# Performance work log

Measured on AMD Instinct MI355X. Metric: run time of the kernel, lower is better.

Reference implementation:

```python
import jax, jax.numpy as jnp
import numpy as np
import math

B, DG, P, DA = 512, 1024, 1024, 256
LN_EPS = 1e-5  # torch LayerNorm default
EPS = 1e-12


def _ln(x, g, b):
    mu = jnp.mean(x, axis=-1, keepdims=True)
    var = jnp.mean((x - mu) ** 2, axis=-1, keepdims=True)
    return (x - mu) * jax.lax.rsqrt(var + LN_EPS) * g + b


def setup_inputs() -> dict:
    key = jax.random.key(0)
    ks = jax.random.split(key, 16)
    s = lambda fan_in: 1.0 / math.sqrt(fan_in)
    return {
        "hg": jax.random.normal(ks[0], (B, DG), jnp.float32),
        "desc_2d": jax.random.normal(ks[1], (B, P), jnp.float32),
        "Wq": jax.random.uniform(ks[2], (DA, DG), jnp.float32, -s(DG), s(DG)),
        "bq": jnp.zeros((DA,), jnp.float32),
        "wk_val": jax.random.uniform(ks[3], (DA,), jnp.float32, -1.0, 1.0),
        "bk_val": jax.random.uniform(ks[4], (DA,), jnp.float32, -1.0, 1.0),
        "wv_val": jax.random.uniform(ks[5], (DA,), jnp.float32, -1.0, 1.0),
        "bv_val": jax.random.uniform(ks[6], (DA,), jnp.float32, -1.0, 1.0),
        "Ek": jax.random.normal(ks[7], (P, DA), jnp.float32),
        "Ev": jax.random.normal(ks[8], (P, DA), jnp.float32),
        "Uq": jax.random.uniform(ks[9], (DA, DA), jnp.float32, -s(DA), s(DA)),
        "Vk": jax.random.uniform(ks[10], (DA, DA), jnp.float32, -s(DA), s(DA)),
        "ln_q_g": jnp.ones((DA,), jnp.float32), "ln_q_b": jnp.zeros((DA,), jnp.float32),
        "ln_k_g": jnp.ones((DA,), jnp.float32), "ln_k_b": jnp.zeros((DA,), jnp.float32),
        "ln_v_g": jnp.ones((DA,), jnp.float32), "ln_v_b": jnp.zeros((DA,), jnp.float32),
    }


def reference(hg, desc_2d, Wq, bq, wk_val, bk_val, wv_val, bv_val, Ek, Ev, Uq, Vk,
              ln_q_g, ln_q_b, ln_k_g, ln_k_b, ln_v_g, ln_v_b):
    # dropout is inference-mode (identity)
    q = _ln(hg @ Wq.T + bq, ln_q_g, ln_q_b)                       # (B, DA)
    # scalar -> token proj plus id embedding
    k = desc_2d[:, :, None] * wk_val + bk_val + Ek[None]          # (B, P, DA)
    v = desc_2d[:, :, None] * wv_val + bv_val + Ev[None]
    k = _ln(k, ln_k_g, ln_k_b)
    v = _ln(v, ln_v_g, ln_v_b)
    q2 = q @ Uq.T                                                 # (B, DA)
    k2 = jnp.einsum('bpd,ed->bpe', k, Vk)                         # (B, P, DA)
    e = jnp.einsum('bpd,bd->bp', k2, q2) / math.sqrt(DA)          # (B, P)
    alpha = jax.nn.sigmoid(e)
    alpha = alpha / (jnp.sum(alpha, axis=1, keepdims=True) + EPS)
    c = jnp.einsum('bp,bpd->bd', alpha, v)                        # (B, DA)
    return c, alpha
```

## Files before the change

kernel.cpp:

```cpp
#include <hip/hip_runtime.h>
#include <math.h>

#define B 512
#define DG 1024
#define P 1024
#define DA 256
#define LDP 68
#define BP (B * P)
#define BD (B * DA)

__device__ __forceinline__ float block_reduce_sum(float v, volatile float* red) {
    #pragma unroll
    for (int off = 32; off > 0; off >>= 1) v += __shfl_down(v, off, 64);
    const int lane = threadIdx.x & 63, wid = threadIdx.x >> 6;
    __syncthreads();
    if (lane == 0) red[wid] = v;
    __syncthreads();
    return red[0] + red[1] + red[2] + red[3];
}
__device__ __forceinline__ float wsum(float v) {
    #pragma unroll
    for (int m = 32; m > 0; m >>= 1) v += __shfl_xor(v, m, 64);
    return v;
}

#define FMA16(a4, b4, acc)                                   \
    acc[0][0] = fmaf(a4.x, b4.x, acc[0][0]);                 \
    acc[0][1] = fmaf(a4.x, b4.y, acc[0][1]);                 \
    acc[0][2] = fmaf(a4.x, b4.z, acc[0][2]);                 \
    acc[0][3] = fmaf(a4.x, b4.w, acc[0][3]);                 \
    acc[1][0] = fmaf(a4.y, b4.x, acc[1][0]);                 \
    acc[1][1] = fmaf(a4.y, b4.y, acc[1][1]);                 \
    acc[1][2] = fmaf(a4.y, b4.z, acc[1][2]);                 \
    acc[1][3] = fmaf(a4.y, b4.w, acc[1][3]);                 \
    acc[2][0] = fmaf(a4.z, b4.x, acc[2][0]);                 \
    acc[2][1] = fmaf(a4.z, b4.y, acc[2][1]);                 \
    acc[2][2] = fmaf(a4.z, b4.z, acc[2][2]);                 \
    acc[2][3] = fmaf(a4.z, b4.w, acc[2][3]);                 \
    acc[3][0] = fmaf(a4.w, b4.x, acc[3][0]);                 \
    acc[3][1] = fmaf(a4.w, b4.y, acc[3][1]);                 \
    acc[3][2] = fmaf(a4.w, b4.z, acc[3][2]);                 \
    acc[3][3] = fmaf(a4.w, b4.w, acc[3][3]);

__device__ __forceinline__ void stage_T(const float* __restrict__ src, int ldk, int m0, int k0,
                                        int tid, float* sD) {
    const int m = tid >> 3, k4 = (tid & 7) * 4;
    #pragma unroll
    for (int pass = 0; pass < 2; ++pass) {
        int mm = m + pass * 32;
        float4 v = *reinterpret_cast<const float4*>(&src[(m0 + mm) * ldk + k0 + k4]);
        sD[(k4 + 0) * LDP + mm] = v.x; sD[(k4 + 1) * LDP + mm] = v.y;
        sD[(k4 + 2) * LDP + mm] = v.z; sD[(k4 + 3) * LDP + mm] = v.w;
    }
}
__device__ __forceinline__ void stage_N1(const float* __restrict__ src, int ldn, int k0, int n0,
                                         int tid, float* sD) {
    const int k = tid >> 4, n4 = (tid & 15) * 4;
    #pragma unroll
    for (int pass = 0; pass < 2; ++pass) {
        int kk = k + pass * 16;
        *reinterpret_cast<float4*>(&sD[kk * LDP + n4]) =
            *reinterpret_cast<const float4*>(&src[(k0 + kk) * ldn + n0 + n4]);
    }
}
__device__ __forceinline__ void mm_inner(const float* sA, const float* sB, int tid, float acc[4][4]) {
    const int ty4 = (tid >> 4) * 4, tx4 = (tid & 15) * 4;
    #pragma unroll
    for (int kk = 0; kk < 32; ++kk) {
        float4 a4 = *reinterpret_cast<const float4*>(&sA[kk * LDP + ty4]);
        float4 b4 = *reinterpret_cast<const float4*>(&sB[kk * LDP + tx4]);
        FMA16(a4, b4, acc)
    }
}

__device__ __forceinline__ void epilog_uw(float dot, float s,
                                          float mck, float Bk, float Ck,
                                          float Bv, float Cv,
                                          float mwk, float Ak, float Av,
                                          float Wg, float Cg, float G_, float Bb,
                                          float& u, float& w) {
    float var = fmaf(s, fmaf(s, Ak, 2.0f * Bk), Ck);
    float rstd = rsqrtf(var + 1e-5f);
    float mu = fmaf(s, mwk, mck);
    float e = (rstd * (fmaf(s, Wg, Cg) + dot - mu * G_) + Bb) * 0.0625f;
    u = 1.0f / (1.0f + expf(-e));
    float varv = fmaf(s, fmaf(s, Av, 2.0f * Bv), Cv);
    w = u * rsqrtf(varv + 1e-5f);
}

__global__ __launch_bounds__(256) void KA(const float* __restrict__ hg, const float* __restrict__ Wq,
                                          const float* __restrict__ Uq,
                                          const float* __restrict__ Ek, const float* __restrict__ Ev,
                                          const float* __restrict__ wk, const float* __restrict__ bk,
                                          const float* __restrict__ wv, const float* __restrict__ bv,
                                          float* __restrict__ qp, float* __restrict__ UqT,
                                          float* __restrict__ pst, float* __restrict__ scal4) {
    __shared__ __align__(16) float sA[32 * LDP];
    __shared__ __align__(16) float sB[32 * LDP];
    const int tid = threadIdx.x, t = blockIdx.x;
    const int ty4 = (tid >> 4) * 4, tx4 = (tid & 15) * 4;

    if (t < 256) {
        const int mt = t & 7, nt = (t >> 3) & 3, ks = t >> 5;
        const int b0 = mt * 64, d0 = nt * 64, kc = ks * 128;
        float acc[4][4] = {};
        for (int kt = 0; kt < 128; kt += 32) {
            stage_T(hg, DG, b0, kc + kt, tid, sA);
            stage_T(Wq, DG, d0, kc + kt, tid, sB);
            __syncthreads();
            mm_inner(sA, sB, tid, acc);
            __syncthreads();
        }
        float* outp = qp + ks * BD;
        #pragma unroll
        for (int i = 0; i < 4; ++i) {
            float4 o = make_float4(acc[i][0], acc[i][1], acc[i][2], acc[i][3]);
            *reinterpret_cast<float4*>(&outp[(b0 + ty4 + i) * DA + d0 + tx4]) = o;
        }
    } else if (t < 320) {
        const int b2 = t - 256;
        const int e0 = (b2 & 7) * 32, f0 = (b2 >> 3) * 32;
        const int col = tid & 31, row8 = tid >> 5;
        #pragma unroll
        for (int pass = 0; pass < 4; ++pass) {
            int r = row8 + pass * 8;
            sA[r * 33 + col] = Uq[(e0 + r) * DA + f0 + col];
        }
        __syncthreads();
        #pragma unroll
        for (int pass = 0; pass < 4; ++pass) {
            int r = row8 + pass * 8;
            UqT[(f0 + r) * DA + e0 + col] = sA[col * 33 + r];
        }
    } else {
        const int tp = t - 320;
        const int wid = tid >> 6, lane = tid & 63;
        const int p = tp * 4 + wid;
        const int d4 = lane * 4;
        const float inv = 1.0f / DA;
        float4 ek4 = *reinterpret_cast<const float4*>(&Ek[p * DA + d4]);
        float4 ev4 = *reinterpret_cast<const float4*>(&Ev[p * DA + d4]);
        float4 wk4 = *reinterpret_cast<const float4*>(&wk[d4]);
        float4 bk4 = *reinterpret_cast<const float4*>(&bk[d4]);
        float4 wv4 = *reinterpret_cast<const float4*>(&wv[d4]);
        float4 bv4 = *reinterpret_cast<const float4*>(&bv[d4]);
        float ck0 = bk4.x + ek4.x, ck1 = bk4.y + ek4.y, ck2 = bk4.z + ek4.z, ck3 = bk4.w + ek4.w;
        float cv0 = bv4.x + ev4.x, cv1 = bv4.y + ev4.y, cv2 = bv4.z + ev4.z, cv3 = bv4.w + ev4.w;
        float Sck  = wsum(ck0 + ck1 + ck2 + ck3);
        float Sck2 = wsum(ck0*ck0 + ck1*ck1 + ck2*ck2 + ck3*ck3);
        float Swck = wsum(wk4.x*ck0 + wk4.y*ck1 + wk4.z*ck2 + wk4.w*ck3);
        float Scv  = wsum(cv0 + cv1 + cv2 + cv3);
        float Scv2 = wsum(cv0*cv0 + cv1*cv1 + cv2*cv2 + cv3*cv3);
        float Swcv = wsum(wv4.x*cv0 + wv4.y*cv1 + wv4.z*cv2 + wv4.w*cv3);
        float Swk  = wsum(wk4.x + wk4.y + wk4.z + wk4.w);
        float Swv  = wsum(wv4.x + wv4.y + wv4.z + wv4.w);
        float mwk = Swk * inv, mwv = Swv * inv;
        float mck = Sck * inv, mcv = Scv * inv;
        if (lane == 0) {
            pst[0 * P + p] = mck;
            pst[1 * P + p] = Swck * inv - mwk * mck;
            pst[2 * P + p] = Sck2 * inv - mck * mck;
            pst[3 * P + p] = mcv;
            pst[4 * P + p] = Swcv * inv - mwv * mcv;
            pst[5 * P + p] = Scv2 * inv - mcv * mcv;
        }
        if (p == 0) {
            float Swk2 = wsum(wk4.x*wk4.x + wk4.y*wk4.y + wk4.z*wk4.z + wk4.w*wk4.w);
            float Swv2 = wsum(wv4.x*wv4.x + wv4.y*wv4.y + wv4.z*wv4.z + wv4.w*wv4.w);
            if (lane == 0) {
                scal4[0] = mwk;
                scal4[1] = Swk2 * inv - mwk * mwk;
                scal4[2] = mwv;
                scal4[3] = Swv2 * inv - mwv * mwv;
            }
        }
    }
}

__global__ __launch_bounds__(256) void KC(const float* __restrict__ qp, const float* __restrict__ bq,
                                          const float* __restrict__ gq, const float* __restrict__ bqln,
                                          const float* __restrict__ UqT, const float* __restrict__ Vk,
                                          const float* __restrict__ gk,
                                          const float* __restrict__ wk, const float* __restrict__ bk,
                                          const float* __restrict__ bkln,
                                          float* __restrict__ gr, float* __restrict__ bscal) {
    __shared__ __align__(16) float q_lds[DA];
    __shared__ __align__(16) float q2_lds[DA];
    __shared__ float red[4];
    const int b = blockIdx.x, d = threadIdx.x;
    float x = bq[d];
    #pragma unroll
    for (int ks = 0; ks < 8; ++ks) x += qp[ks * BD + b * DA + d];
    float mu = block_reduce_sum(x, red) * (1.0f / DA);
    float xc = x - mu;
    float var = block_reduce_sum(xc * xc, red) * (1.0f / DA);
    float qv = xc * rsqrtf(var + 1e-5f) * gq[d] + bqln[d];
    q_lds[d] = qv;
    __syncthreads();

    float q2 = 0.f;
    for (int f = 0; f < DA; f += 4) {
        float4 qf = *reinterpret_cast<const float4*>(&q_lds[f]);
        q2 = fmaf(qf.x, UqT[(f + 0) * DA + d], q2);
        q2 = fmaf(qf.y, UqT[(f + 1) * DA + d], q2);
        q2 = fmaf(qf.z, UqT[(f + 2) * DA + d], q2);
        q2 = fmaf(qf.w, UqT[(f + 3) * DA + d], q2);
    }
    q2_lds[d] = q2;
    __syncthreads();

    float r = 0.f;
    for (int e = 0; e < DA; e += 4) {
        float4 qe = *reinterpret_cast<const float4*>(&q2_lds[e]);
        r = fmaf(qe.x, Vk[(e + 0) * DA + d], r);
        r = fmaf(qe.y, Vk[(e + 1) * DA + d], r);
        r = fmaf(qe.z, Vk[(e + 2) * DA + d], r);
        r = fmaf(qe.w, Vk[(e + 3) * DA + d], r);
    }
    float grv = gk[d] * r;
    gr[b * DA + d] = grv;

    float Wg = block_reduce_sum(wk[d] * grv, red);
    float Cg = block_reduce_sum(bk[d] * grv, red);
    float G_ = block_reduce_sum(grv, red);
    float Bb = block_reduce_sum(bkln[d] * r, red);
    if (d == 0) {
        bscal[b] = Wg; bscal[B + b] = Cg;
        bscal[2 * B + b] = G_; bscal[3 * B + b] = Bb;
    }
}

__global__ __launch_bounds__(256) void KD(const float* __restrict__ gr, const float* __restrict__ Ek,
                                          float* __restrict__ epart) {
    __shared__ __align__(16) float sA[32 * LDP];
    __shared__ __align__(16) float sB[32 * LDP];
    const int tid = threadIdx.x, t = blockIdx.x;
    const int ty4 = (tid >> 4) * 4, tx4 = (tid & 15) * 4;
    const int mt = t & 7, nt = (t >> 3) & 15, ks = t >> 7;
    const int b0 = mt * 64, p0 = nt * 64, kc = ks * 128;
    float acc[4][4] = {};
    for (int kt = 0; kt < 128; kt += 32) {
        stage_T(gr, DA, b0, kc + kt, tid, sA);
        stage_T(Ek, DA, p0, kc + kt, tid, sB);
        __syncthreads();
        mm_inner(sA, sB, tid, acc);
        __syncthreads();
    }
    float* outp = epart + ks * BP;
    #pragma unroll
    for (int i = 0; i < 4; ++i) {
        float4 o = make_float4(acc[i][0], acc[i][1], acc[i][2], acc[i][3]);
        *reinterpret_cast<float4*>(&outp[(b0 + ty4 + i) * P + p0 + tx4]) = o;
    }
}

__global__ __launch_bounds__(256) void KF(const float* __restrict__ epart, const float* __restrict__ desc,
                                          const float* __restrict__ bscal, const float* __restrict__ pst,
                                          const float* __restrict__ scal4, const float* __restrict__ Ev,
                                          float* __restrict__ cpart) {
    __shared__ __align__(16) float sA[32 * LDP];
    __shared__ __align__(16) float sB[32 * LDP];
    const int tid = threadIdx.x, t = blockIdx.x;
    const int ty4 = (tid >> 4) * 4, tx4 = (tid & 15) * 4;
    const int mt = t & 7, nt = (t >> 3) & 3, ks = t >> 5;
    const int b0 = mt * 64, d0 = nt * 64, kc = ks * 128;
    const float mwk = scal4[0], Ak = scal4[1], Av = scal4[3];
    const int m = tid >> 3, k4 = (tid & 7) * 4;
    float acc[4][4] = {};
    for (int kt = 0; kt < 128; kt += 32) {
        const int kg = kc + kt;
        #pragma unroll
        for (int pass = 0; pass < 2; ++pass) {
            int mm = m + pass * 32;
            const int b = b0 + mm;
            const int p = kg + k4;
            float4 e0 = *reinterpret_cast<const float4*>(&epart[b * P + p]);
            float4 e1 = *reinterpret_cast<const float4*>(&epart[BP + b * P + p]);
            float4 s4 = *reinterpret_cast<const float4*>(&desc[b * P + p]);
            float4 mck4 = *reinterpret_cast<const float4*>(&pst[p]);
            float4 Bk4  = *reinterpret_cast<const float4*>(&pst[P + p]);
            float4 Ck4  = *reinterpret_cast<const float4*>(&pst[2 * P + p]);
            float4 Bv4  = *reinterpret_cast<const float4*>(&pst[4 * P + p]);
            float4 Cv4  = *reinterpret_cast<const float4*>(&pst[5 * P + p]);
            const float Wg = bscal[b], Cg = bscal[B + b];
            const float G_ = bscal[2 * B + b], Bb = bscal[3 * B + b];
            float u, w;
            epilog_uw(e0.x + e1.x, s4.x, mck4.x, Bk4.x, Ck4.x, Bv4.x, Cv4.x,
                      mwk, Ak, Av, Wg, Cg, G_, Bb, u, w);
            sA[(k4 + 0) * LDP + mm] = w;
            epilog_uw(e0.y + e1.y, s4.y, mck4.y, Bk4.y, Ck4.y, Bv4.y, Cv4.y,
                      mwk, Ak, Av, Wg, Cg, G_, Bb, u, w);
            sA[(k4 + 1) * LDP + mm] = w;
            epilog_uw(e0.z + e1.z, s4.z, mck4.z, Bk4.z, Ck4.z, Bv4.z, Cv4.z,
                      mwk, Ak, Av, Wg, Cg, G_, Bb, u, w);
            sA[(k4 + 2) * LDP + mm] = w;
            epilog_uw(e0.w + e1.w, s4.w, mck4.w, Bk4.w, Ck4.w, Bv4.w, Cv4.w,
                      mwk, Ak, Av, Wg, Cg, G_, Bb, u, w);
            sA[(k4 + 3) * LDP + mm] = w;
        }
        stage_N1(Ev, DA, kg, d0, tid, sB);
        __syncthreads();
        mm_inner(sA, sB, tid, acc);
        __syncthreads();
    }
    float* outp = cpart + ks * BD;
    #pragma unroll
    for (int i = 0; i < 4; ++i) {
        float4 o = make_float4(acc[i][0], acc[i][1], acc[i][2], acc[i][3]);
        *reinterpret_cast<float4*>(&outp[(b0 + ty4 + i) * DA + d0 + tx4]) = o;
    }
}

__global__ __launch_bounds__(256) void KG(const float* __restrict__ epart, const float* __restrict__ desc,
                                          const float* __restrict__ bscal, const float* __restrict__ pst,
                                          const float* __restrict__ scal4, const float* __restrict__ cpart,
                                          const float* __restrict__ gv, const float* __restrict__ wv,
                                          const float* __restrict__ bvv, const float* __restrict__ bvln,
                                          float* __restrict__ alpha_out, float* __restrict__ out_c) {
    __shared__ float red[4];
    const int b = blockIdx.x, tid = threadIdx.x;
    const float mwk = scal4[0], Ak = scal4[1], mwv = scal4[2], Av = scal4[3];
    const float Wg = bscal[b], Cg = bscal[B + b], G_ = bscal[2 * B + b], Bb = bscal[3 * B + b];
    float u[4];
    float us = 0.f, ws_ = 0.f, wss = 0.f, wms = 0.f;
    #pragma unroll
    for (int j = 0; j < 4; ++j) {
        int p = j * 256 + tid;
        float dot = epart[b * P + p] + epart[BP + b * P + p];
        float s = desc[b * P + p];
        float uu, ww;
        epilog_uw(dot, s, pst[p], pst[P + p], pst[2 * P + p], pst[4 * P + p], pst[5 * P + p],
                  mwk, Ak, Av, Wg, Cg, G_, Bb, uu, ww);
        u[j] = uu;
        us += uu; ws_ += ww;
        wss = fmaf(ww, s, wss);
        wms = fmaf(ww, fmaf(s, mwv, pst[3 * P + p]), wms);
    }
    float S   = block_reduce_sum(us, red);
    float SB  = block_reduce_sum(ws_, red);
    float SBs = block_reduce_sum(wss, red);
    float SBm = block_reduce_sum(wms, red);
    float invS = 1.0f / (S + 1e-12f);
    float T = S * invS;
    #pragma unroll
    for (int j = 0; j < 4; ++j)
        alpha_out[b * P + j * 256 + tid] = u[j] * invS;
    const int d = tid;
    float csum = 0.f;
    #pragma unroll
    for (int ks = 0; ks < 8; ++ks) csum += cpart[ks * BD + b * DA + d];
    out_c[b * DA + d] =
        invS * (gv[d] * (wv[d] * SBs + bvv[d] * SB + csum - SBm)) + bvln[d] * T;
}

extern "C" void kernel_launch(void* const* d_in, const int* in_sizes, int n_in,
                              void* d_out, int out_size, void* d_ws, size_t ws_size,
                              hipStream_t stream) {
    (void)in_sizes; (void)n_in; (void)out_size; (void)ws_size;
    const float* hg   = (const float*)d_in[0];
    const float* desc = (const float*)d_in[1];
    const float* Wq   = (const float*)d_in[2];
    const float* bq   = (const float*)d_in[3];
    const float* wk   = (const float*)d_in[4];
    const float* bk   = (const float*)d_in[5];
    const float* wv   = (const float*)d_in[6];
    const float* bv   = (const float*)d_in[7];
    const float* Ek   = (const float*)d_in[8];
    const float* Ev   = (const float*)d_in[9];
    const float* Uq   = (const float*)d_in[10];
    const float* Vk   = (const float*)d_in[11];
    const float* gq   = (const float*)d_in[12];
    const float* bqln = (const float*)d_in[13];
    const float* gk   = (const float*)d_in[14];
    const float* bkln = (const float*)d_in[15];
    const float* gv   = (const float*)d_in[16];
    const float* bvln = (const float*)d_in[17];

    float* out = (float*)d_out;
    float* out_c = out;
    float* out_alpha = out + BD;

    float* ws = (float*)d_ws;
    float* qp    = ws;
    float* UqT   = ws + 1048576;
    float* gr    = ws + 1114112;
    float* epart = ws + 1245184;
    float* cpart = ws + 2293760;
    float* bscal = ws + 3342336;
    float* pst   = ws + 3344384;
    float* scal4 = ws + 3350528;

    KA<<<576, 256, 0, stream>>>(hg, Wq, Uq, Ek, Ev, wk, bk, wv, bv, qp, UqT, pst, scal4);
    KC<<<512, 256, 0, stream>>>(qp, bq, gq, bqln, UqT, Vk, gk, wk, bk, bkln, gr, bscal);
    KD<<<256, 256, 0, stream>>>(gr, Ek, epart);
    KF<<<256, 256, 0, stream>>>(epart, desc, bscal, pst, scal4, Ev, cpart);
    KG<<<512, 256, 0, stream>>>(epart, desc, bscal, pst, scal4, cpart, gv, wv, bv, bvln,
                                out_alpha, out_c);
}
```

Before: 57.52 us.

## Precompose Uq and gk-scaled Vk into one matrix and fold reduction vectors

Rather than running two chained 256x256 matvecs per batch row in KC (q·Uq, then ·Vk, then gk scaling), KA now precomputes M = Uq^T·diag-scaled Vk as a split-K GEMM with two partial outputs. It also precomputes four projection vectors so the per-row scalars (Wg, Cg, G, Bb) become dot products with q. KC then does a single matvec over M (summing the two partials on load) plus four reductions, which removes one sequential matvec and a barrier. The cost is extra one-off weight work in KA, including a single serial block for the vectors, and a change in the order of floating-point summation.

New measurement: 70.47 us. 1.23x slower.

```diff
diff --git a/kernel.cpp b/kernel.cpp
--- a/kernel.cpp
+++ b/kernel.cpp
@@ -89,12 +89,14 @@
 }
 
 __global__ __launch_bounds__(256) void KA(const float* __restrict__ hg, const float* __restrict__ Wq,
-                                          const float* __restrict__ Uq,
+                                          const float* __restrict__ Uq, const float* __restrict__ Vk,
                                           const float* __restrict__ Ek, const float* __restrict__ Ev,
                                           const float* __restrict__ wk, const float* __restrict__ bk,
                                           const float* __restrict__ wv, const float* __restrict__ bv,
-                                          float* __restrict__ qp, float* __restrict__ UqT,
-                                          float* __restrict__ pst, float* __restrict__ scal4) {
+                                          const float* __restrict__ gk, const float* __restrict__ bkln,
+                                          float* __restrict__ qp, float* __restrict__ Mp,
+                                          float* __restrict__ pst, float* __restrict__ scal4,
+                                          float* __restrict__ vec4) {
     __shared__ __align__(16) float sA[32 * LDP];
     __shared__ __align__(16) float sB[32 * LDP];
     const int tid = threadIdx.x, t = blockIdx.x;
@@ -117,23 +119,79 @@
             float4 o = make_float4(acc[i][0], acc[i][1], acc[i][2], acc[i][3]);
             *reinterpret_cast<float4*>(&outp[(b0 + ty4 + i) * DA + d0 + tx4]) = o;
         }
-    } else if (t < 320) {
-        const int b2 = t - 256;
-        const int e0 = (b2 & 7) * 32, f0 = (b2 >> 3) * 32;
-        const int col = tid & 31, row8 = tid >> 5;
+    } else if (t < 288) {
+        const int t2 = t - 256;
+        const int ft = t2 & 3, dt = (t2 >> 2) & 3, ks = t2 >> 4;
+        const int f0 = ft * 64, d0 = dt * 64, kc = ks * 128;
+        const int k = tid >> 4, n4 = (tid & 15) * 4;
+        float acc[4][4] = {};
+        for (int kt = 0; kt < 128; kt += 32) {
+            const int kg = kc + kt;
+            stage_N1(Uq, DA, kg, f0, tid, sA);
+            float4 g = *reinterpret_cast<const float4*>(&gk[d0 + n4]);
+            #pragma unroll
+            for (int pass = 0; pass < 2; ++pass) {
+                int kk = k + pass * 16;
+                float4 v = *reinterpret_cast<const float4*>(&Vk[(kg + kk) * DA + d0 + n4]);
+                v.x *= g.x; v.y *= g.y; v.z *= g.z; v.w *= g.w;
+                *reinterpret_cast<float4*>(&sB[kk * LDP + n4]) = v;
+            }
+            __syncthreads();
+            mm_inner(sA, sB, tid, acc);
+            __syncthreads();
+        }
+        float* outp = Mp + ks * (DA * DA);
         #pragma unroll
-        for (int pass = 0; pass < 4; ++pass) {
-            int r = row8 + pass * 8;
-            sA[r * 33 + col] = Uq[(e0 + r) * DA + f0 + col];
-        }
-        __syncthreads();
-        #pragma unroll
-        for (int pass = 0; pass < 4; ++pass) {
-            int r = row8 + pass * 8;
-            UqT[(f0 + r) * DA + e0 + col] = sA[col * 33 + r];
-        }
+        for (int i = 0; i < 4; ++i) {
+            float4 o = make_float4(acc[i][0], acc[i][1], acc[i][2], acc[i][3]);
+            *reinterpret_cast<float4*>(&outp[(f0 + ty4 + i) * DA + d0 + tx4]) = o;
+        }
+    } else if (t == 288) {
+        float* w4  = sA;
+        float* tmp = sB;
+        float gkd = gk[tid];
+        w4[0 * 256 + tid] = wk[tid] * gkd;
+        w4[1 * 256 + tid] = bk[tid] * gkd;
+        w4[2 * 256 + tid] = gkd;
+        w4[3 * 256 + tid] = bkln[tid];
+        __syncthreads();
+        const int dl = tid & 15, eg = tid >> 4;
+        for (int eb = 0; eb < 16; ++eb) {
+            int e = eb * 16 + eg;
+            float p0 = 0.f, p1 = 0.f, p2 = 0.f, p3 = 0.f;
+            #pragma unroll
+            for (int tt = 0; tt < 16; ++tt) {
+                int d = dl + tt * 16;
+                float v = Vk[e * DA + d];
+                p0 = fmaf(v, w4[d], p0);
+                p1 = fmaf(v, w4[256 + d], p1);
+                p2 = fmaf(v, w4[512 + d], p2);
+                p3 = fmaf(v, w4[768 + d], p3);
+            }
+            #pragma unroll
+            for (int m = 8; m > 0; m >>= 1) {
+                p0 += __shfl_xor(p0, m, 16);
+                p1 += __shfl_xor(p1, m, 16);
+                p2 += __shfl_xor(p2, m, 16);
+                p3 += __shfl_xor(p3, m, 16);
+            }
+            if (dl == 0) {
+                tmp[e * 4 + 0] = p0; tmp[e * 4 + 1] = p1;
+                tmp[e * 4 + 2] = p2; tmp[e * 4 + 3] = p3;
+            }
+        }
+        __syncthreads();
+        float a0 = 0.f, a1 = 0.f, a2 = 0.f, a3 = 0.f;
+        for (int e = 0; e < 256; ++e) {
+            float u = Uq[e * DA + tid];
+            a0 = fmaf(u, tmp[e * 4 + 0], a0);
+            a1 = fmaf(u, tmp[e * 4 + 1], a1);
+            a2 = fmaf(u, tmp[e * 4 + 2], a2);
+            a3 = fmaf(u, tmp[e * 4 + 3], a3);
+        }
+        vec4[tid] = a0; vec4[256 + tid] = a1; vec4[512 + tid] = a2; vec4[768 + tid] = a3;
     } else {
-        const int tp = t - 320;
+        const int tp = t - 289;
         const int wid = tid >> 6, lane = tid & 63;
         const int p = tp * 4 + wid;
         const int d4 = lane * 4;
@@ -179,13 +237,9 @@
 
 __global__ __launch_bounds__(256) void KC(const float* __restrict__ qp, const float* __restrict__ bq,
                                           const float* __restrict__ gq, const float* __restrict__ bqln,
-                                          const float* __restrict__ UqT, const float* __restrict__ Vk,
-                                          const float* __restrict__ gk,
-                                          const float* __restrict__ wk, const float* __restrict__ bk,
-                                          const float* __restrict__ bkln,
+                                          const float* __restrict__ vec4, const float* __restrict__ Mp,
                                           float* __restrict__ gr, float* __restrict__ bscal) {
     __shared__ __align__(16) float q_lds[DA];
-    __shared__ __align__(16) float q2_lds[DA];
     __shared__ float red[4];
     const int b = blockIdx.x, d = threadIdx.x;
     float x = bq[d];
@@ -196,38 +250,25 @@
     float var = block_reduce_sum(xc * xc, red) * (1.0f / DA);
     float qv = xc * rsqrtf(var + 1e-5f) * gq[d] + bqln[d];
     q_lds[d] = qv;
-    __syncthreads();
-
-    float q2 = 0.f;
-    for (int f = 0; f < DA; f += 4) {
-        float4 qf = *reinterpret_cast<const float4*>(&q_lds[f]);
-        q2 = fmaf(qf.x, UqT[(f + 0) * DA + d], q2);
-        q2 = fmaf(qf.y, UqT[(f + 1) * DA + d], q2);
-        q2 = fmaf(qf.z, UqT[(f + 2) * DA + d], q2);
-        q2 = fmaf(qf.w, UqT[(f + 3) * DA + d], q2);
-    }
-    q2_lds[d] = q2;
-    __syncthreads();
-
-    float r = 0.f;
-    for (int e = 0; e < DA; e += 4) {
-        float4 qe = *reinterpret_cast<const float4*>(&q2_lds[e]);
-        r = fmaf(qe.x, Vk[(e + 0) * DA + d], r);
-        r = fmaf(qe.y, Vk[(e + 1) * DA + d], r);
-        r = fmaf(qe.z, Vk[(e + 2) * DA + d], r);
-        r = fmaf(qe.w, Vk[(e + 3) * DA + d], r);
-    }
-    float grv = gk[d] * r;
-    gr[b * DA + d] = grv;
-
-    float Wg = block_reduce_sum(wk[d] * grv, red);
-    float Cg = block_reduce_sum(bk[d] * grv, red);
-    float G_ = block_reduce_sum(grv, red);
-    float Bb = block_reduce_sum(bkln[d] * r, red);
+    float Wg = block_reduce_sum(qv * vec4[d], red);
+    float Cg = block_reduce_sum(qv * vec4[256 + d], red);
+    float G_ = block_reduce_sum(qv * vec4[512 + d], red);
+    float Bb = block_reduce_sum(qv * vec4[768 + d], red);
     if (d == 0) {
         bscal[b] = Wg; bscal[B + b] = Cg;
         bscal[2 * B + b] = G_; bscal[3 * B + b] = Bb;
     }
+    const float* M0 = Mp;
+    const float* M1 = Mp + DA * DA;
+    float grv = 0.f;
+    for (int f = 0; f < DA; f += 4) {
+        float4 qf = *reinterpret_cast<const float4*>(&q_lds[f]);
+        grv = fmaf(qf.x, M0[(f + 0) * DA + d] + M1[(f + 0) * DA + d], grv);
+        grv = fmaf(qf.y, M0[(f + 1) * DA + d] + M1[(f + 1) * DA + d], grv);
+        grv = fmaf(qf.z, M0[(f + 2) * DA + d] + M1[(f + 2) * DA + d], grv);
+        grv = fmaf(qf.w, M0[(f + 3) * DA + d] + M1[(f + 3) * DA + d], grv);
+    }
+    gr[b * DA + d] = grv;
 }
 
 __global__ __launch_bounds__(256) void KD(const float* __restrict__ gr, const float* __restrict__ Ek,
@@ -382,16 +423,18 @@
 
     float* ws = (float*)d_ws;
     float* qp    = ws;
-    float* UqT   = ws + 1048576;
-    float* gr    = ws + 1114112;
-    float* epart = ws + 1245184;
-    float* cpart = ws + 2293760;
-    float* bscal = ws + 3342336;
-    float* pst   = ws + 3344384;
-    float* scal4 = ws + 3350528;
-
-    KA<<<576, 256, 0, stream>>>(hg, Wq, Uq, Ek, Ev, wk, bk, wv, bv, qp, UqT, pst, scal4);
-    KC<<<512, 256, 0, stream>>>(qp, bq, gq, bqln, UqT, Vk, gk, wk, bk, bkln, gr, bscal);
+    float* Mp    = ws + 1048576;
+    float* gr    = ws + 1179648;
+    float* epart = ws + 1310720;
+    float* cpart = ws + 2359296;
+    float* vec4  = ws + 3407872;
+    float* bscal = ws + 3408896;
+    float* pst   = ws + 3410944;
+    float* scal4 = ws + 3417088;
+
+    KA<<<545, 256, 0, stream>>>(hg, Wq, Uq, Vk, Ek, Ev, wk, bk, wv, bv, gk, bkln,
+                                qp, Mp, pst, scal4, vec4);
+    KC<<<512, 256, 0, stream>>>(qp, bq, gq, bqln, vec4, Mp, gr, bscal);
     KD<<<256, 256, 0, stream>>>(gr, Ek, epart);
     KF<<<256, 256, 0, stream>>>(epart, desc, bscal, pst, scal4, Ev, cpart);
     KG<<<512, 256, 0, stream>>>(epart, desc, bscal, pst, scal4, cpart, gv, wv, bv, bvln,
```
